# Optimization experiments

Hardware: AMD Instinct MI355X
Metric: run time of the kernel (lower is better)

Reference implementation:

```python
import jax, jax.numpy as jnp
import numpy as np

N_NODES = 100000
N_EDGES = 1600000
N_GRAPHS = 64
EPS = 1e-16  # matches PyG softmax eps


def _glorot(key, shape):
    fan_in, fan_out = shape[0], shape[1]
    lim = np.sqrt(6.0 / (fan_in + fan_out))
    return jax.random.uniform(key, shape, jnp.float32, -lim, lim)


def setup_inputs() -> dict:
    key = jax.random.key(0)
    ks = jax.random.split(key, 20)
    x = jax.random.normal(ks[0], (N_NODES, 3), jnp.float32)
    edge_index = jax.random.randint(ks[1], (2, N_EDGES), 0, N_NODES, jnp.int64)
    batch = jnp.sort(jax.random.randint(ks[2], (N_NODES,), 0, N_GRAPHS, jnp.int64))
    p = {
        # gat1: TransformerConv(3 -> 32, heads=2, concat) => H*D = 64
        'Wq1': _glorot(ks[3], (3, 64)),  'bq1': jnp.zeros((64,), jnp.float32),
        'Wk1': _glorot(ks[4], (3, 64)),  'bk1': jnp.zeros((64,), jnp.float32),
        'Wv1': _glorot(ks[5], (3, 64)),  'bv1': jnp.zeros((64,), jnp.float32),
        'Ws1': _glorot(ks[6], (3, 64)),  'bs1': jnp.zeros((64,), jnp.float32),
        # gat2: TransformerConv(64 -> 64, heads=2, concat) => H*D = 128
        'Wq2': _glorot(ks[7], (64, 128)), 'bq2': jnp.zeros((128,), jnp.float32),
        'Wk2': _glorot(ks[8], (64, 128)), 'bk2': jnp.zeros((128,), jnp.float32),
        'Wv2': _glorot(ks[9], (64, 128)), 'bv2': jnp.zeros((128,), jnp.float32),
        'Ws2': _glorot(ks[10], (64, 128)), 'bs2': jnp.zeros((128,), jnp.float32),
        # MLP head
        'W1': _glorot(ks[11], (128, 32)),  'b1': jnp.zeros((32,), jnp.float32),
        'W2': _glorot(ks[12], (32, 128)),  'b2': jnp.zeros((128,), jnp.float32),
        'W3': _glorot(ks[13], (128, 40)),  'b3': jnp.zeros((40,), jnp.float32),
    }
    return {'x': x, 'edge_index': edge_index, 'batch': batch, **p}


def transformer_conv(x, src, dst, Wq, bq, Wk, bk, Wv, bv, Ws, bs, heads, d):
    """PyG TransformerConv (concat=True, root_weight=True, no edge_attr, no beta)."""
    n = x.shape[0]
    q = (x @ Wq + bq).reshape(n, heads, d)
    k = (x @ Wk + bk).reshape(n, heads, d)
    v = (x @ Wv + bv).reshape(n, heads, d)
    # gather per edge: query at target (i = dst), key/value at source (j = src)
    logits = jnp.einsum('ehd,ehd->eh', q[dst], k[src]) / jnp.sqrt(jnp.float32(d))  # [E,H]
    # segment softmax over incoming edges of each target node
    m = jax.ops.segment_max(logits, dst, num_segments=n)          # [N,H]
    m = jnp.where(jnp.isfinite(m), m, 0.0)
    e = jnp.exp(logits - m[dst])                                   # [E,H]
    s = jax.ops.segment_sum(e, dst, num_segments=n)                # [N,H]
    alpha = e / (s[dst] + EPS)                                     # [E,H]
    out = jax.ops.segment_sum(alpha[:, :, None] * v[src], dst, num_segments=n)  # [N,H,D]
    out = out.reshape(n, heads * d)
    return out + (x @ Ws + bs)  # skip connection (root_weight)


def global_max_pool(x, batch, num_graphs):
    return jax.ops.segment_max(x, batch, num_segments=num_graphs)


def reference(x, edge_index, batch,
              Wq1, bq1, Wk1, bk1, Wv1, bv1, Ws1, bs1,
              Wq2, bq2, Wk2, bk2, Wv2, bv2, Ws2, bs2,
              W1, b1, W2, b2, W3, b3):
    src, dst = edge_index[0], edge_index[1]
    h = jax.nn.relu(transformer_conv(x, src, dst, Wq1, bq1, Wk1, bk1, Wv1, bv1, Ws1, bs1, heads=2, d=32))
    h = jax.nn.relu(transformer_conv(h, src, dst, Wq2, bq2, Wk2, bk2, Wv2, bv2, Ws2, bs2, heads=2, d=64))
    g = global_max_pool(h, batch, N_GRAPHS)            # [G,128]
    latent = jax.nn.relu(g @ W1 + b1)                   # [G,32]
    h2 = jax.nn.relu(latent @ W2 + b2)                  # [G,128]
    logits = h2 @ W3 + b3                               # [G,40]
    return (logits, latent)
```

## Files before the change

### kernel.cpp

```cpp
#include <hip/hip_runtime.h>
#include <hip/hip_bf16.h>

typedef __hip_bfloat16 bf16;
typedef unsigned short u16;
typedef unsigned int u32;
typedef __attribute__((ext_vector_type(8))) short bf16x8;
typedef __attribute__((ext_vector_type(4))) float f32x4;
typedef __attribute__((ext_vector_type(2))) float f32x2;

#define NN 100000
#define NE 1600000
#define NG 64
#define NBKT 196
#define EPB 4096
#define NBLK ((NE + EPB - 1) / EPB)

__device__ __forceinline__ float ldf(const void* __restrict__ p, int i, int isbf) {
    return isbf ? __bfloat162float(((const bf16*)p)[i]) : ((const float*)p)[i];
}

__device__ __forceinline__ int ld_idx(const int* __restrict__ p, int i, int is64) {
    return is64 ? p[2 * i] : p[i];
}

__device__ __forceinline__ u16 f2bu(float f) {
    u32 u = __float_as_uint(f);
    u32 r = u + 0x7fffu + ((u >> 16) & 1u);
    return (u16)(r >> 16);
}
__device__ __forceinline__ float blo(u32 u) { return __uint_as_float(u << 16); }
__device__ __forceinline__ float bhi(u32 u) { return __uint_as_float(u & 0xffff0000u); }

__global__ void k_detect(const int* __restrict__ ei, const int* __restrict__ bat,
                         const u16* __restrict__ xw, int* __restrict__ flags) {
    __shared__ int anyE, anyB, cntF;
    if (threadIdx.x == 0) { anyE = 0; anyB = 0; cntF = 0; }
    __syncthreads();
    int t = threadIdx.x;
    int accE = 0, accB = 0;
#pragma unroll
    for (int i = 0; i < 8; i++) {
        int si = t * 8 + i;
        long long pe = ((long long)si * (2LL * NE)) / 2048;
        int ie = ((int)pe) | 1;
        if (ie < 2 * NE) accE |= ei[ie];
    }
    {
        int ib = (int)(((long long)t * NN) / 256) | 1;
        if (ib < NN) accB |= bat[ib];
    }
    if (accE) atomicOr(&anyE, 1);
    if (accB) atomicOr(&anyB, 1);
    {
        u16 w = xw[2 * t];
        int hb = (w >> 8) & 0x7F;
        if (hb >= 0x3B && hb <= 0x41) atomicAdd(&cntF, 1);
    }
    __syncthreads();
    if (threadIdx.x == 0) {
        flags[0] = anyE ? 0 : 1;
        flags[1] = anyB ? 0 : 1;
        flags[2] = (cntF > 128) ? 1 : 0;
    }
}

__global__ void k_p1hist(const int* __restrict__ ei, const int* __restrict__ flags,
                         int* __restrict__ bhistT) {
    __shared__ int lh[NBKT];
    int t = threadIdx.x;
    if (t < NBKT) lh[t] = 0;
    __syncthreads();
    int is64 = flags[0];
    int base = blockIdx.x * EPB;
#pragma unroll
    for (int i = 0; i < EPB / 512; i++) {
        int e = base + i * 512 + t;
        if (e < NE) {
            int di = ld_idx(ei, NE + e, is64);
            atomicAdd(&lh[di >> 9], 1);
        }
    }
    __syncthreads();
    if (t < NBKT) bhistT[t * NBLK + blockIdx.x] = lh[t];
}

__global__ void k_p2a(const int* __restrict__ bhistT, int* __restrict__ boffT,
                      int* __restrict__ btot) {
    __shared__ int sh[512];
    int b = blockIdx.x, t = threadIdx.x;
    int v = (t < NBLK) ? bhistT[b * NBLK + t] : 0;
    sh[t] = v;
    __syncthreads();
#pragma unroll
    for (int off = 1; off < 512; off <<= 1) {
        int y = (t >= off) ? sh[t - off] : 0;
        __syncthreads();
        sh[t] += y;
        __syncthreads();
    }
    if (t < NBLK) boffT[b * NBLK + t] = sh[t] - v;
    if (t == 511) btot[b] = sh[511];
}

__global__ void k_p2b(const int* __restrict__ btot, int* __restrict__ bbase) {
    __shared__ int sh[256];
    int t = threadIdx.x;
    int v = (t < NBKT) ? btot[t] : 0;
    sh[t] = v;
    __syncthreads();
#pragma unroll
    for (int off = 1; off < 256; off <<= 1) {
        int y = (t >= off) ? sh[t - off] : 0;
        __syncthreads();
        sh[t] += y;
        __syncthreads();
    }
    if (t < NBKT) bbase[t] = sh[t] - v;
    if (t == 255) bbase[NBKT] = sh[255];
}

__global__ void k_p3part(const int* __restrict__ ei, const int* __restrict__ flags,
                         const int* __restrict__ boffT, const int* __restrict__ bbase,
                         u32* __restrict__ pairs) {
    __shared__ int loff[NBKT];
    int t = threadIdx.x;
    if (t < NBKT) loff[t] = bbase[t] + boffT[t * NBLK + blockIdx.x];
    __syncthreads();
    int is64 = flags[0];
    int base = blockIdx.x * EPB;
#pragma unroll
    for (int i = 0; i < EPB / 512; i++) {
        int e = base + i * 512 + t;
        if (e < NE) {
            int sj = ld_idx(ei, e, is64);
            int di = ld_idx(ei, NE + e, is64);
            int pos = atomicAdd(&loff[di >> 9], 1);
            pairs[pos] = ((u32)sj << 9) | (u32)(di & 511);
        }
    }
}

__global__ void k_p4sort(const u32* __restrict__ pairs, const int* __restrict__ bbase,
                         int* __restrict__ rowptr, int* __restrict__ es) {
    __shared__ int lcnt[512], pfx[512];
    int b = blockIdx.x, t = threadIdx.x;
    int bb = bbase[b];
    int bend = bbase[b + 1];
    int n0 = b << 9;
    lcnt[t] = 0;
    __syncthreads();
    for (int p = bb + t; p < bend; p += 512)
        atomicAdd(&lcnt[pairs[p] & 511u], 1);
    __syncthreads();
    int v = lcnt[t];
    pfx[t] = v;
    __syncthreads();
#pragma unroll
    for (int off = 1; off < 512; off <<= 1) {
        int y = (t >= off) ? pfx[t - off] : 0;
        __syncthreads();
        pfx[t] += y;
        __syncthreads();
    }
    int start = bb + pfx[t] - v;
    int n = n0 + t;
    if (n < NN) rowptr[n] = start;
    lcnt[t] = start;
    if (b == NBKT - 1 && t == 0) rowptr[NN] = NE;
    __syncthreads();
    for (int p = bb + t; p < bend; p += 512) {
        u32 pr = pairs[p];
        int pos = atomicAdd(&lcnt[pr & 511u], 1);
        es[pos] = (int)(pr >> 9);
    }
}

__global__ void k_qkvs1(const void* __restrict__ x,
                        const void* __restrict__ Wq, const void* __restrict__ bq,
                        const void* __restrict__ Wk, const void* __restrict__ bk,
                        const void* __restrict__ Wv, const void* __restrict__ bv,
                        const void* __restrict__ Ws, const void* __restrict__ bs,
                        const int* __restrict__ flags,
                        u16* __restrict__ q1b, u16* __restrict__ kv1m,
                        u16* __restrict__ s1b) {
    int idx = blockIdx.x * blockDim.x + threadIdx.x;
    if (idx >= NN * 64) return;
    int fb = flags[2];
    int n = idx >> 6, d = idx & 63;
    float x0 = ldf(x, n * 3 + 0, fb);
    float x1 = ldf(x, n * 3 + 1, fb);
    float x2 = ldf(x, n * 3 + 2, fb);
    q1b[idx] = f2bu(x0 * ldf(Wq, d, fb) + x1 * ldf(Wq, 64 + d, fb) + x2 * ldf(Wq, 128 + d, fb) + ldf(bq, d, fb));
    s1b[idx] = f2bu(x0 * ldf(Ws, d, fb) + x1 * ldf(Ws, 64 + d, fb) + x2 * ldf(Ws, 128 + d, fb) + ldf(bs, d, fb));
    float kf = x0 * ldf(Wk, d, fb) + x1 * ldf(Wk, 64 + d, fb) + x2 * ldf(Wk, 128 + d, fb) + ldf(bk, d, fb);
    float vf = x0 * ldf(Wv, d, fb) + x1 * ldf(Wv, 64 + d, fb) + x2 * ldf(Wv, 128 + d, fb) + ldf(bv, d, fb);
    float knb = __shfl_xor(kf, 1, 64);
    if (!(d & 1)) {
        int packed = __builtin_amdgcn_cvt_pk_fp8_f32(kf, knb, 0, false);
        kv1m[(size_t)n * 96 + (d >> 1)] = (u16)packed;
    }
    kv1m[(size_t)n * 96 + 32 + d] = f2bu(vf);
}

__global__ void k_attn1(const int* __restrict__ rowptr, const int* __restrict__ es,
                        const u16* __restrict__ q1b, const u16* __restrict__ kv1m,
                        const u16* __restrict__ s1b, u16* __restrict__ h1b) {
    int w = (blockIdx.x * blockDim.x + threadIdx.x) >> 6;
    if (w >= NN) return;
    int lane = threadIdx.x & 63;
    int g = lane >> 4, hl = lane & 15;
    const float scale = 0.17677669529663687f;
    uint2 qu = ((const uint2*)(q1b + (size_t)w * 64))[hl];
    float qs0 = blo(qu.x) * scale, qs1 = bhi(qu.x) * scale;
    float qs2 = blo(qu.y) * scale, qs3 = bhi(qu.y) * scale;
    float l = 0.0f, o0 = 0.0f, o1 = 0.0f, o2 = 0.0f, o3 = 0.0f;
    int beg = rowptr[w], end = rowptr[w + 1];
    int iters = (end - beg + 3) >> 2;
#define PROC1(ku, vu, vld) { \
    f32x2 k01 = __builtin_amdgcn_cvt_pk_f32_fp8((int)ku, false); \
    f32x2 k23 = __builtin_amdgcn_cvt_pk_f32_fp8((int)ku, true); \
    float t = qs0 * k01.x + qs1 * k01.y + qs2 * k23.x + qs3 * k23.y; \
    t += __shfl_xor(t, 4, 64); t += __shfl_xor(t, 2, 64); t += __shfl_xor(t, 1, 64); \
    float e = (vld) ? __expf(t) : 0.0f; \
    l += e; \
    o0 += e * blo(vu.x); o1 += e * bhi(vu.x); \
    o2 += e * blo(vu.y); o3 += e * bhi(vu.y); }
    if (iters > 0) {
        int pA = beg + g;
        int vA = pA < end; int sjA = es[vA ? pA : beg];
        u32 kA = *(const u32*)(kv1m + (size_t)sjA * 96 + hl * 2);
        uint2 uA = *(const uint2*)(kv1m + (size_t)sjA * 96 + 32 + hl * 4);
        int pB = pA + 4;
        int vB = pB < end; int sjB = es[vB ? pB : beg];
        u32 kB = *(const u32*)(kv1m + (size_t)sjB * 96 + hl * 2);
        uint2 uB = *(const uint2*)(kv1m + (size_t)sjB * 96 + 32 + hl * 4);
        int pC = pA + 8;
        int vC = pC < end; int sjC = es[vC ? pC : beg];
        u32 kC = *(const u32*)(kv1m + (size_t)sjC * 96 + hl * 2);
        uint2 uC = *(const uint2*)(kv1m + (size_t)sjC * 96 + 32 + hl * 4);
        for (int i = 0; i < iters; i += 3) {
            int pD = pA + 12;
            int vD = pD < end; int sjD = es[vD ? pD : beg];
            u32 kD = *(const u32*)(kv1m + (size_t)sjD * 96 + hl * 2);
            uint2 uD = *(const uint2*)(kv1m + (size_t)sjD * 96 + 32 + hl * 4);
            PROC1(kA, uA, vA);
            int pE = pA + 16;
            int vE = pE < end; int sjE = es[vE ? pE : beg];
            u32 kE = *(const u32*)(kv1m + (size_t)sjE * 96 + hl * 2);
            uint2 uE = *(const uint2*)(kv1m + (size_t)sjE * 96 + 32 + hl * 4);
            PROC1(kB, uB, vB);
            int pF = pA + 20;
            int vF = pF < end; int sjF = es[vF ? pF : beg];
            u32 kF = *(const u32*)(kv1m + (size_t)sjF * 96 + hl * 2);
            uint2 uF = *(const uint2*)(kv1m + (size_t)sjF * 96 + 32 + hl * 4);
            PROC1(kC, uC, vC);
            pA = pD; vA = vD; kA = kD; uA = uD;
            pB = pE; vB = vE; kB = kE; uB = uE;
            pC = pF; vC = vF; kC = kF; uC = uF;
        }
    }
#undef PROC1
#pragma unroll
    for (int off = 16; off <= 32; off <<= 1) {
        l += __shfl_xor(l, off, 64);
        o0 += __shfl_xor(o0, off, 64);
        o1 += __shfl_xor(o1, off, 64);
        o2 += __shfl_xor(o2, off, 64);
        o3 += __shfl_xor(o3, off, 64);
    }
    if (g == 0) {
        float inv = 1.0f / (l + 1e-16f);
        uint2 su = ((const uint2*)(s1b + (size_t)w * 64))[hl];
        uint2 r;
        r.x = (u32)f2bu(fmaxf(blo(su.x) + o0 * inv, 0.0f)) | ((u32)f2bu(fmaxf(bhi(su.x) + o1 * inv, 0.0f)) << 16);
        r.y = (u32)f2bu(fmaxf(blo(su.y) + o2 * inv, 0.0f)) | ((u32)f2bu(fmaxf(bhi(su.y) + o3 * inv, 0.0f)) << 16);
        ((uint2*)(h1b + (size_t)w * 64))[hl] = r;
    }
}

__global__ void k_wprep(const void* __restrict__ Wq, const void* __restrict__ bq,
                        const void* __restrict__ Wk, const void* __restrict__ bk,
                        const void* __restrict__ Wv, const void* __restrict__ bv,
                        const void* __restrict__ Ws, const void* __restrict__ bs,
                        const int* __restrict__ flags,
                        u16* __restrict__ Wt, float* __restrict__ bias,
                        float* __restrict__ g) {
    int idx = blockIdx.x * blockDim.x + threadIdx.x;
    if (idx >= 512 * 64) return;
    if (idx < NG * 128) g[idx] = 0.0f;
    int fb = flags[2];
    int n = idx >> 6, k = idx & 63;
    int mat = n >> 7, c = n & 127;
    const void* W = (mat == 0) ? Wq : (mat == 1) ? Wk : (mat == 2) ? Wv : Ws;
    Wt[n * 64 + k] = f2bu(ldf(W, k * 128 + c, fb));
    if (k == 0) {
        const void* B = (mat == 0) ? bq : (mat == 1) ? bk : (mat == 2) ? bv : bs;
        bias[n] = ldf(B, c, fb);
    }
}

__global__ void k_gemm2(const u16* __restrict__ h1b, const u16* __restrict__ Wt,
                        const float* __restrict__ bias,
                        u16* __restrict__ q2b, u16* __restrict__ kvm,
                        u16* __restrict__ s2b) {
    int w = (blockIdx.x * blockDim.x + threadIdx.x) >> 6;
    if (w >= NN / 16) return;
    int lane = threadIdx.x & 63;
    int quad = lane >> 4, mr = lane & 15;
    int m0 = w * 16;
    const u16* arow = h1b + (size_t)(m0 + mr) * 64 + quad * 8;
    bf16x8 a0 = *(const bf16x8*)(arow);
    bf16x8 a1 = *(const bf16x8*)(arow + 32);
#pragma unroll 4
    for (int n0 = 0; n0 < 512; n0 += 16) {
        const u16* brow = Wt + (size_t)(n0 + mr) * 64 + quad * 8;
        bf16x8 b0 = *(const bf16x8*)(brow);
        bf16x8 b1 = *(const bf16x8*)(brow + 32);
        f32x4 acc = {0.f, 0.f, 0.f, 0.f};
        acc = __builtin_amdgcn_mfma_f32_16x16x32_bf16(a0, b0, acc, 0, 0, 0);
        acc = __builtin_amdgcn_mfma_f32_16x16x32_bf16(a1, b1, acc, 0, 0, 0);
        float bs = bias[n0 + mr];
        int mat = n0 >> 7;
        int c = (n0 & 127) + mr;
#pragma unroll
        for (int r = 0; r < 4; r++) {
            int row = m0 + quad * 4 + r;
            float val = acc[r] + bs;
            if (mat == 1) {
                float nb = __shfl_xor(val, 1, 64);
                if (!(mr & 1)) {
                    int packed = __builtin_amdgcn_cvt_pk_fp8_f32(val, nb, 0, false);
                    *(u16*)((char*)kvm + (size_t)row * 384 + c) = (u16)packed;
                }
            } else if (mat == 0) {
                q2b[(size_t)row * 128 + c] = f2bu(val);
            } else if (mat == 2) {
                kvm[(size_t)row * 192 + 64 + c] = f2bu(val);
            } else {
                s2b[(size_t)row * 128 + c] = f2bu(val);
            }
        }
    }
}

__global__ void k_attn2(const int* __restrict__ rowptr, const int* __restrict__ es,
                        const u16* __restrict__ q2b, const u16* __restrict__ kvm,
                        const u16* __restrict__ s2b, u16* __restrict__ h2b) {
    int w = (blockIdx.x * blockDim.x + threadIdx.x) >> 6;
    if (w >= NN) return;
    int lane = threadIdx.x & 63;
    int g = lane >> 4, hl = lane & 15;
    const float scale = 0.125f;
    uint4 qu = ((const uint4*)(q2b + (size_t)w * 128))[hl];
    float qs[8];
    qs[0] = blo(qu.x) * scale; qs[1] = bhi(qu.x) * scale;
    qs[2] = blo(qu.y) * scale; qs[3] = bhi(qu.y) * scale;
    qs[4] = blo(qu.z) * scale; qs[5] = bhi(qu.z) * scale;
    qs[6] = blo(qu.w) * scale; qs[7] = bhi(qu.w) * scale;
    float l = 0.0f;
    float o[8] = {0.f, 0.f, 0.f, 0.f, 0.f, 0.f, 0.f, 0.f};
    int beg = rowptr[w], end = rowptr[w + 1];
    int iters = (end - beg + 3) >> 2;
#define PROC2(ku, vu, vld) { \
    f32x2 k01 = __builtin_amdgcn_cvt_pk_f32_fp8((int)ku.x, false); \
    f32x2 k23 = __builtin_amdgcn_cvt_pk_f32_fp8((int)ku.x, true); \
    f32x2 k45 = __builtin_amdgcn_cvt_pk_f32_fp8((int)ku.y, false); \
    f32x2 k67 = __builtin_amdgcn_cvt_pk_f32_fp8((int)ku.y, true); \
    float t = qs[0] * k01.x + qs[1] * k01.y + qs[2] * k23.x + qs[3] * k23.y \
            + qs[4] * k45.x + qs[5] * k45.y + qs[6] * k67.x + qs[7] * k67.y; \
    t += __shfl_xor(t, 4, 64); t += __shfl_xor(t, 2, 64); t += __shfl_xor(t, 1, 64); \
    float e = (vld) ? __expf(t) : 0.0f; \
    l += e; \
    o[0] += e * blo(vu.x); o[1] += e * bhi(vu.x); \
    o[2] += e * blo(vu.y); o[3] += e * bhi(vu.y); \
    o[4] += e * blo(vu.z); o[5] += e * bhi(vu.z); \
    o[6] += e * blo(vu.w); o[7] += e * bhi(vu.w); }
    if (iters > 0) {
        int pA = beg + g;
        int vA = pA < end; int sjA = es[vA ? pA : beg];
        uint2 kA = ((const uint2*)(kvm + (size_t)sjA * 192))[hl];
        uint4 uA = ((const uint4*)(kvm + (size_t)sjA * 192 + 64))[hl];
        int pB = pA + 4;
        int vB = pB < end; int sjB = es[vB ? pB : beg];
        uint2 kB = ((const uint2*)(kvm + (size_t)sjB * 192))[hl];
        uint4 uB = ((const uint4*)(kvm + (size_t)sjB * 192 + 64))[hl];
        int pC = pA + 8;
        int vC = pC < end; int sjC = es[vC ? pC : beg];
        uint2 kC = ((const uint2*)(kvm + (size_t)sjC * 192))[hl];
        uint4 uC = ((const uint4*)(kvm + (size_t)sjC * 192 + 64))[hl];
        for (int i = 0; i < iters; i += 3) {
            int pD = pA + 12;
            int vD = pD < end; int sjD = es[vD ? pD : beg];
            uint2 kD = ((const uint2*)(kvm + (size_t)sjD * 192))[hl];
            uint4 uD = ((const uint4*)(kvm + (size_t)sjD * 192 + 64))[hl];
            PROC2(kA, uA, vA);
            int pE = pA + 16;
            int vE = pE < end; int sjE = es[vE ? pE : beg];
            uint2 kE = ((const uint2*)(kvm + (size_t)sjE * 192))[hl];
            uint4 uE = ((const uint4*)(kvm + (size_t)sjE * 192 + 64))[hl];
            PROC2(kB, uB, vB);
            int pF = pA + 20;
            int vF = pF < end; int sjF = es[vF ? pF : beg];
            uint2 kF = ((const uint2*)(kvm + (size_t)sjF * 192))[hl];
            uint4 uF = ((const uint4*)(kvm + (size_t)sjF * 192 + 64))[hl];
            PROC2(kC, uC, vC);
            pA = pD; vA = vD; kA = kD; uA = uD;
            pB = pE; vB = vE; kB = kE; uB = uE;
            pC = pF; vC = vF; kC = kF; uC = uF;
        }
    }
#undef PROC2
#pragma unroll
    for (int off = 16; off <= 32; off <<= 1) {
        l += __shfl_xor(l, off, 64);
#pragma unroll
        for (int j = 0; j < 8; j++) o[j] += __shfl_xor(o[j], off, 64);
    }
    if (g == 0) {
        float inv = 1.0f / (l + 1e-16f);
        uint4 su = ((const uint4*)(s2b + (size_t)w * 128))[hl];
        uint4 r;
        r.x = (u32)f2bu(blo(su.x) + o[0] * inv) | ((u32)f2bu(bhi(su.x) + o[1] * inv) << 16);
        r.y = (u32)f2bu(blo(su.y) + o[2] * inv) | ((u32)f2bu(bhi(su.y) + o[3] * inv) << 16);
        r.z = (u32)f2bu(blo(su.z) + o[4] * inv) | ((u32)f2bu(bhi(su.z) + o[5] * inv) << 16);
        r.w = (u32)f2bu(blo(su.w) + o[6] * inv) | ((u32)f2bu(bhi(su.w) + o[7] * inv) << 16);
        ((uint4*)(h2b + (size_t)w * 128))[hl] = r;
    }
}

__global__ void k_pool(const u16* __restrict__ h2b, const int* __restrict__ batch,
                       const int* __restrict__ flags, float* __restrict__ g) {
    int idx = blockIdx.x * blockDim.x + threadIdx.x;
    if (idx >= (NN / 16) * 128) return;
    int is64 = flags[1];
    int d = idx & 127, ch = idx >> 7;
    int n0 = ch * 16;
    int curb = ld_idx(batch, n0, is64);
    float mx = 0.0f;
    for (int i = 0; i < 16; i++) {
        int n = n0 + i;
        int b = ld_idx(batch, n, is64);
        if (b != curb) {
            atomicMax((int*)&g[curb * 128 + d], __float_as_int(mx));
            mx = 0.0f;
            curb = b;
        }
        mx = fmaxf(mx, __uint_as_float(((u32)h2b[(size_t)n * 128 + d]) << 16));
    }
    atomicMax((int*)&g[curb * 128 + d], __float_as_int(mx));
}

__global__ void k_mlp(const float* __restrict__ g,
                      const void* __restrict__ W1, const void* __restrict__ b1,
                      const void* __restrict__ W2, const void* __restrict__ b2,
                      const void* __restrict__ W3, const void* __restrict__ b3,
                      const int* __restrict__ flags, float* __restrict__ out) {
    __shared__ float gr[128], lat[32], h2[128];
    int gid = blockIdx.x, t = threadIdx.x;
    int fb = flags[2];
    gr[t] = g[gid * 128 + t];
    __syncthreads();
    if (t < 32) {
        float a = ldf(b1, t, fb);
        for (int k = 0; k < 128; k++) a += gr[k] * ldf(W1, k * 32 + t, fb);
        a = fmaxf(a, 0.0f);
        lat[t] = a;
        out[NG * 40 + gid * 32 + t] = a;
    }
    __syncthreads();
    {
        float a = ldf(b2, t, fb);
        for (int k = 0; k < 32; k++) a += lat[k] * ldf(W2, k * 128 + t, fb);
        h2[t] = fmaxf(a, 0.0f);
    }
    __syncthreads();
    if (t < 40) {
        float a = ldf(b3, t, fb);
        for (int k = 0; k < 128; k++) a += h2[k] * ldf(W3, k * 40 + t, fb);
        out[gid * 40 + t] = a;
    }
}

extern "C" void kernel_launch(void* const* d_in, const int* in_sizes, int n_in,
                              void* d_out, int out_size, void* d_ws, size_t ws_size,
                              hipStream_t stream) {
    const void* x     = d_in[0];
    const int*  ei    = (const int*)d_in[1];
    const int*  batch = (const int*)d_in[2];
    const void *Wq1 = d_in[3],  *bq1 = d_in[4];
    const void *Wk1 = d_in[5],  *bk1 = d_in[6];
    const void *Wv1 = d_in[7],  *bv1 = d_in[8];
    const void *Ws1 = d_in[9],  *bs1 = d_in[10];
    const void *Wq2 = d_in[11], *bq2 = d_in[12];
    const void *Wk2 = d_in[13], *bk2 = d_in[14];
    const void *Wv2 = d_in[15], *bv2 = d_in[16];
    const void *Ws2 = d_in[17], *bs2 = d_in[18];
    const void *W1  = d_in[19], *b1  = d_in[20];
    const void *W2  = d_in[21], *b2  = d_in[22];
    const void *W3  = d_in[23], *b3  = d_in[24];

    float* ws = (float*)d_ws;
    float* g    = ws;
    float* bias = g + NG * 128;
    u16* u16base = (u16*)(bias + 512);
    u16* kvm   = u16base;
    u16* kv1m  = kvm + (size_t)NN * 192;
    u16* h1b   = kv1m + (size_t)NN * 96;
    u16* q1b   = h1b + (size_t)NN * 64;
    u16* s1b   = q1b + (size_t)NN * 64;
    u16* q2b   = s1b + (size_t)NN * 64;
    u16* s2b   = q2b + (size_t)NN * 128;
    u16* h2b   = s2b + (size_t)NN * 128;
    u16* Wt    = h2b + (size_t)NN * 128;
    int* flags  = (int*)(Wt + 512 * 64);
    int* rowptr = flags + 8;
    int* bhistT = rowptr + NN + 1;
    int* boffT  = bhistT + NBKT * NBLK;
    int* btot   = boffT + NBKT * NBLK;
    int* bbase  = btot + NBKT;
    int* es     = bbase + NBKT + 1;
    u32* pairs = (u32*)kvm;

    float* out  = (float*)d_out;

    const int B = 256;
    k_detect<<<1, 256, 0, stream>>>(ei, batch, (const u16*)x, flags);
    k_p1hist<<<NBLK, 512, 0, stream>>>(ei, flags, bhistT);
    k_p2a<<<NBKT, 512, 0, stream>>>(bhistT, boffT, btot);
    k_p2b<<<1, 256, 0, stream>>>(btot, bbase);
    k_p3part<<<NBLK, 512, 0, stream>>>(ei, flags, boffT, bbase, pairs);
    k_p4sort<<<NBKT, 512, 0, stream>>>(pairs, bbase, rowptr, es);
    k_qkvs1<<<(NN * 64 + B - 1) / B, B, 0, stream>>>(x, Wq1, bq1, Wk1, bk1, Wv1, bv1, Ws1, bs1,
                                                     flags, q1b, kv1m, s1b);
    k_attn1<<<(NN * 64 + B - 1) / B, B, 0, stream>>>(rowptr, es, q1b, kv1m, s1b, h1b);
    k_wprep<<<(512 * 64 + B - 1) / B, B, 0, stream>>>(Wq2, bq2, Wk2, bk2, Wv2, bv2, Ws2, bs2,
                                                      flags, Wt, bias, g);
    k_gemm2<<<(NN / 16 * 64 + B - 1) / B, B, 0, stream>>>(h1b, Wt, bias, q2b, kvm, s2b);
    k_attn2<<<(NN * 64 + B - 1) / B, B, 0, stream>>>(rowptr, es, q2b, kvm, s2b, h2b);
    k_pool<<<((NN / 16) * 128 + B - 1) / B, B, 0, stream>>>(h2b, batch, flags, g);
    k_mlp<<<NG, 128, 0, stream>>>(g, W1, b1, W2, b2, W3, b3, flags, out);
}
```

Measured before the change: 435.6 us.

## Fuse small launches and cut gather prefetch depth in attention kernels

Removes the separate detect, p2b and wprep launches. Index-width detection now runs per block inside the histogram and partition kernels, the final bucket scan runs in the last-arriving p2a block via an atomic ticket, and the layer-2 weight prep is folded into extra blocks of the qkvs1 launch. The aim is fewer kernel launches and fewer serialization points. Both attention kernels also drop from 3-deep to 2-deep software prefetch of neighbor K/V rows, which lowers register pressure but gives less latency hiding; the ticket scheme also adds atomics and fences.

```diff
diff --git a/kernel.cpp b/kernel.cpp
--- a/kernel.cpp
+++ b/kernel.cpp
@@ -14,6 +14,8 @@
 #define NBKT 196
 #define EPB 4096
 #define NBLK ((NE + EPB - 1) / EPB)
+#define QB 25000
+#define WB 128
 
 __device__ __forceinline__ float ldf(const void* __restrict__ p, int i, int isbf) {
     return isbf ? __bfloat162float(((const bf16*)p)[i]) : ((const float*)p)[i];
@@ -31,47 +33,30 @@
 __device__ __forceinline__ float blo(u32 u) { return __uint_as_float(u << 16); }
 __device__ __forceinline__ float bhi(u32 u) { return __uint_as_float(u & 0xffff0000u); }
 
-__global__ void k_detect(const int* __restrict__ ei, const int* __restrict__ bat,
-                         const u16* __restrict__ xw, int* __restrict__ flags) {
-    __shared__ int anyE, anyB, cntF;
-    if (threadIdx.x == 0) { anyE = 0; anyB = 0; cntF = 0; }
-    __syncthreads();
+__device__ __forceinline__ int block_detect_is64(const int* __restrict__ ei, int base,
+                                                 int* s_any) {
     int t = threadIdx.x;
-    int accE = 0, accB = 0;
-#pragma unroll
-    for (int i = 0; i < 8; i++) {
-        int si = t * 8 + i;
-        long long pe = ((long long)si * (2LL * NE)) / 2048;
-        int ie = ((int)pe) | 1;
-        if (ie < 2 * NE) accE |= ei[ie];
-    }
-    {
-        int ib = (int)(((long long)t * NN) / 256) | 1;
-        if (ib < NN) accB |= bat[ib];
-    }
-    if (accE) atomicOr(&anyE, 1);
-    if (accB) atomicOr(&anyB, 1);
-    {
-        u16 w = xw[2 * t];
-        int hb = (w >> 8) & 0x7F;
-        if (hb >= 0x3B && hb <= 0x41) atomicAdd(&cntF, 1);
-    }
-    __syncthreads();
-    if (threadIdx.x == 0) {
-        flags[0] = anyE ? 0 : 1;
-        flags[1] = anyB ? 0 : 1;
-        flags[2] = (cntF > 128) ? 1 : 0;
-    }
-}
-
-__global__ void k_p1hist(const int* __restrict__ ei, const int* __restrict__ flags,
+    int acc = 0;
+    int w0 = 2 * base + 4 * t + 1;
+    int w1 = 2 * base + 4 * t + 3;
+    if (w0 < 2 * NE) acc |= ei[w0];
+    if (w1 < 2 * NE) acc |= ei[w1];
+    if (acc) atomicOr(s_any, 1);
+    __syncthreads();
+    return *s_any ? 0 : 1;
+}
+
+__global__ void k_p1hist(const int* __restrict__ ei, const int* __restrict__ bat,
+                         const u16* __restrict__ xw, int* __restrict__ flags,
                          int* __restrict__ bhistT) {
     __shared__ int lh[NBKT];
+    __shared__ int s_any, s_anyB, s_cntF;
     int t = threadIdx.x;
     if (t < NBKT) lh[t] = 0;
-    __syncthreads();
-    int is64 = flags[0];
+    if (t == 0) { s_any = 0; s_anyB = 0; s_cntF = 0; }
+    __syncthreads();
     int base = blockIdx.x * EPB;
+    int is64 = block_detect_is64(ei, base, &s_any);
 #pragma unroll
     for (int i = 0; i < EPB / 512; i++) {
         int e = base + i * 512 + t;
@@ -80,13 +65,27 @@
             atomicAdd(&lh[di >> 9], 1);
         }
     }
+    if (blockIdx.x == 0 && t < 256) {
+        int ib = (int)(((long long)t * NN) / 256) | 1;
+        if (ib < NN && bat[ib]) atomicOr(&s_anyB, 1);
+        u16 w = xw[2 * t];
+        int hb = (w >> 8) & 0x7F;
+        if (hb >= 0x3B && hb <= 0x41) atomicAdd(&s_cntF, 1);
+    }
     __syncthreads();
     if (t < NBKT) bhistT[t * NBLK + blockIdx.x] = lh[t];
+    if (blockIdx.x == 0 && t == 0) {
+        flags[1] = s_anyB ? 0 : 1;
+        flags[2] = (s_cntF > 128) ? 1 : 0;
+        flags[4] = 0;
+    }
 }
 
 __global__ void k_p2a(const int* __restrict__ bhistT, int* __restrict__ boffT,
-                      int* __restrict__ btot) {
+                      int* __restrict__ btot, int* __restrict__ ticket,
+                      int* __restrict__ bbase) {
     __shared__ int sh[512];
+    __shared__ int s_last;
     int b = blockIdx.x, t = threadIdx.x;
     int v = (t < NBLK) ? bhistT[b * NBLK + t] : 0;
     sh[t] = v;
@@ -99,35 +98,42 @@
         __syncthreads();
     }
     if (t < NBLK) boffT[b * NBLK + t] = sh[t] - v;
-    if (t == 511) btot[b] = sh[511];
-}
-
-__global__ void k_p2b(const int* __restrict__ btot, int* __restrict__ bbase) {
-    __shared__ int sh[256];
-    int t = threadIdx.x;
-    int v = (t < NBKT) ? btot[t] : 0;
-    sh[t] = v;
-    __syncthreads();
-#pragma unroll
-    for (int off = 1; off < 256; off <<= 1) {
-        int y = (t >= off) ? sh[t - off] : 0;
+    if (t == 511) {
+        atomicExch(&btot[b], sh[511]);
+        __threadfence();
+    }
+    __syncthreads();
+    if (t == 0) s_last = (atomicAdd(ticket, 1) == NBKT - 1) ? 1 : 0;
+    __syncthreads();
+    if (s_last) {
+        __threadfence();
+        int vv = (t < NBKT) ? atomicAdd(&btot[t], 0) : 0;
         __syncthreads();
-        sh[t] += y;
+        sh[t] = vv;
         __syncthreads();
-    }
-    if (t < NBKT) bbase[t] = sh[t] - v;
-    if (t == 255) bbase[NBKT] = sh[255];
-}
-
-__global__ void k_p3part(const int* __restrict__ ei, const int* __restrict__ flags,
+#pragma unroll
+        for (int off = 1; off < 512; off <<= 1) {
+            int y = (t >= off) ? sh[t - off] : 0;
+            __syncthreads();
+            sh[t] += y;
+            __syncthreads();
+        }
+        if (t < NBKT) bbase[t] = sh[t] - vv;
+        if (t == 511) bbase[NBKT] = sh[511];
+    }
+}
+
+__global__ void k_p3part(const int* __restrict__ ei,
                          const int* __restrict__ boffT, const int* __restrict__ bbase,
                          u32* __restrict__ pairs) {
     __shared__ int loff[NBKT];
+    __shared__ int s_any;
     int t = threadIdx.x;
     if (t < NBKT) loff[t] = bbase[t] + boffT[t * NBLK + blockIdx.x];
-    __syncthreads();
-    int is64 = flags[0];
+    if (t == 0) s_any = 0;
+    __syncthreads();
     int base = blockIdx.x * EPB;
+    int is64 = block_detect_is64(ei, base, &s_any);
 #pragma unroll
     for (int i = 0; i < EPB / 512; i++) {
         int e = base + i * 512 + t;
@@ -180,12 +186,30 @@
                         const void* __restrict__ Wk, const void* __restrict__ bk,
                         const void* __restrict__ Wv, const void* __restrict__ bv,
                         const void* __restrict__ Ws, const void* __restrict__ bs,
+                        const void* __restrict__ Wq2, const void* __restrict__ bq2,
+                        const void* __restrict__ Wk2, const void* __restrict__ bk2,
+                        const void* __restrict__ Wv2, const void* __restrict__ bv2,
+                        const void* __restrict__ Ws2, const void* __restrict__ bs2,
                         const int* __restrict__ flags,
                         u16* __restrict__ q1b, u16* __restrict__ kv1m,
-                        u16* __restrict__ s1b) {
+                        u16* __restrict__ s1b,
+                        u16* __restrict__ Wt, float* __restrict__ bias,
+                        float* __restrict__ g) {
+    int fb = flags[2];
+    if (blockIdx.x >= QB) {
+        int idx = (blockIdx.x - QB) * 256 + threadIdx.x;
+        if (idx < NG * 128) g[idx] = 0.0f;
+        int n = idx >> 6, k = idx & 63;
+        int mat = n >> 7, c = n & 127;
+        const void* W = (mat == 0) ? Wq2 : (mat == 1) ? Wk2 : (mat == 2) ? Wv2 : Ws2;
+        Wt[n * 64 + k] = f2bu(ldf(W, k * 128 + c, fb));
+        if (k == 0) {
+            const void* B = (mat == 0) ? bq2 : (mat == 1) ? bk2 : (mat == 2) ? bv2 : bs2;
+            bias[n] = ldf(B, c, fb);
+        }
+        return;
+    }
     int idx = blockIdx.x * blockDim.x + threadIdx.x;
-    if (idx >= NN * 64) return;
-    int fb = flags[2];
     int n = idx >> 6, d = idx & 63;
     float x0 = ldf(x, n * 3 + 0, fb);
     float x1 = ldf(x, n * 3 + 1, fb);
@@ -234,29 +258,19 @@
         int vB = pB < end; int sjB = es[vB ? pB : beg];
         u32 kB = *(const u32*)(kv1m + (size_t)sjB * 96 + hl * 2);
         uint2 uB = *(const uint2*)(kv1m + (size_t)sjB * 96 + 32 + hl * 4);
-        int pC = pA + 8;
-        int vC = pC < end; int sjC = es[vC ? pC : beg];
-        u32 kC = *(const u32*)(kv1m + (size_t)sjC * 96 + hl * 2);
-        uint2 uC = *(const uint2*)(kv1m + (size_t)sjC * 96 + 32 + hl * 4);
-        for (int i = 0; i < iters; i += 3) {
+        for (int i = 0; i < iters; i += 2) {
+            int pC = pA + 8;
+            int vC = pC < end; int sjC = es[vC ? pC : beg];
+            u32 kC = *(const u32*)(kv1m + (size_t)sjC * 96 + hl * 2);
+            uint2 uC = *(const uint2*)(kv1m + (size_t)sjC * 96 + 32 + hl * 4);
+            PROC1(kA, uA, vA);
             int pD = pA + 12;
             int vD = pD < end; int sjD = es[vD ? pD : beg];
             u32 kD = *(const u32*)(kv1m + (size_t)sjD * 96 + hl * 2);
             uint2 uD = *(const uint2*)(kv1m + (size_t)sjD * 96 + 32 + hl * 4);
-            PROC1(kA, uA, vA);
-            int pE = pA + 16;
-            int vE = pE < end; int sjE = es[vE ? pE : beg];
-            u32 kE = *(const u32*)(kv1m + (size_t)sjE * 96 + hl * 2);
-            uint2 uE = *(const uint2*)(kv1m + (size_t)sjE * 96 + 32 + hl * 4);
             PROC1(kB, uB, vB);
-            int pF = pA + 20;
-            int vF = pF < end; int sjF = es[vF ? pF : beg];
-            u32 kF = *(const u32*)(kv1m + (size_t)sjF * 96 + hl * 2);
-            uint2 uF = *(const uint2*)(kv1m + (size_t)sjF * 96 + 32 + hl * 4);
-            PROC1(kC, uC, vC);
-            pA = pD; vA = vD; kA = kD; uA = uD;
-            pB = pE; vB = vE; kB = kE; uB = uE;
-            pC = pF; vC = vF; kC = kF; uC = uF;
+            pA = pC; vA = vC; kA = kC; uA = uC;
+            pB = pD; vB = vD; kB = kD; uB = uD;
         }
     }
 #undef PROC1
@@ -275,27 +289,6 @@
         r.x = (u32)f2bu(fmaxf(blo(su.x) + o0 * inv, 0.0f)) | ((u32)f2bu(fmaxf(bhi(su.x) + o1 * inv, 0.0f)) << 16);
         r.y = (u32)f2bu(fmaxf(blo(su.y) + o2 * inv, 0.0f)) | ((u32)f2bu(fmaxf(bhi(su.y) + o3 * inv, 0.0f)) << 16);
         ((uint2*)(h1b + (size_t)w * 64))[hl] = r;
-    }
-}
-
-__global__ void k_wprep(const void* __restrict__ Wq, const void* __restrict__ bq,
-                        const void* __restrict__ Wk, const void* __restrict__ bk,
-                        const void* __restrict__ Wv, const void* __restrict__ bv,
-                        const void* __restrict__ Ws, const void* __restrict__ bs,
-                        const int* __restrict__ flags,
-                        u16* __restrict__ Wt, float* __restrict__ bias,
-                        float* __restrict__ g) {
-    int idx = blockIdx.x * blockDim.x + threadIdx.x;
-    if (idx >= 512 * 64) return;
-    if (idx < NG * 128) g[idx] = 0.0f;
-    int fb = flags[2];
-    int n = idx >> 6, k = idx & 63;
-    int mat = n >> 7, c = n & 127;
-    const void* W = (mat == 0) ? Wq : (mat == 1) ? Wk : (mat == 2) ? Wv : Ws;
-    Wt[n * 64 + k] = f2bu(ldf(W, k * 128 + c, fb));
-    if (k == 0) {
-        const void* B = (mat == 0) ? bq : (mat == 1) ? bk : (mat == 2) ? bv : bs;
-        bias[n] = ldf(B, c, fb);
     }
 }
 
@@ -384,29 +377,19 @@
         int vB = pB < end; int sjB = es[vB ? pB : beg];
         uint2 kB = ((const uint2*)(kvm + (size_t)sjB * 192))[hl];
         uint4 uB = ((const uint4*)(kvm + (size_t)sjB * 192 + 64))[hl];
-        int pC = pA + 8;
-        int vC = pC < end; int sjC = es[vC ? pC : beg];
-        uint2 kC = ((const uint2*)(kvm + (size_t)sjC * 192))[hl];
-        uint4 uC = ((const uint4*)(kvm + (size_t)sjC * 192 + 64))[hl];
-        for (int i = 0; i < iters; i += 3) {
+        for (int i = 0; i < iters; i += 2) {
+            int pC = pA + 8;
+            int vC = pC < end; int sjC = es[vC ? pC : beg];
+            uint2 kC = ((const uint2*)(kvm + (size_t)sjC * 192))[hl];
+            uint4 uC = ((const uint4*)(kvm + (size_t)sjC * 192 + 64))[hl];
+            PROC2(kA, uA, vA);
             int pD = pA + 12;
             int vD = pD < end; int sjD = es[vD ? pD : beg];
             uint2 kD = ((const uint2*)(kvm + (size_t)sjD * 192))[hl];
             uint4 uD = ((const uint4*)(kvm + (size_t)sjD * 192 + 64))[hl];
-            PROC2(kA, uA, vA);
-            int pE = pA + 16;
-            int vE = pE < end; int sjE = es[vE ? pE : beg];
-            uint2 kE = ((const uint2*)(kvm + (size_t)sjE * 192))[hl];
-            uint4 uE = ((const uint4*)(kvm + (size_t)sjE * 192 + 64))[hl];
             PROC2(kB, uB, vB);
-            int pF = pA + 20;
-            int vF = pF < end; int sjF = es[vF ? pF : beg];
-            uint2 kF = ((const uint2*)(kvm + (size_t)sjF * 192))[hl];
-            uint4 uF = ((const uint4*)(kvm + (size_t)sjF * 192 + 64))[hl];
-            PROC2(kC, uC, vC);
-            pA = pD; vA = vD; kA = kD; uA = uD;
-            pB = pE; vB = vE; kB = kE; uB = uE;
-            pC = pF; vC = vF; kC = kF; uC = uF;
+            pA = pC; vA = vC; kA = kC; uA = uC;
+            pB = pD; vB = vD; kB = kD; uB = uD;
         }
     }
 #undef PROC2
@@ -524,17 +507,14 @@
     float* out  = (float*)d_out;
 
     const int B = 256;
-    k_detect<<<1, 256, 0, stream>>>(ei, batch, (const u16*)x, flags);
-    k_p1hist<<<NBLK, 512, 0, stream>>>(ei, flags, bhistT);
-    k_p2a<<<NBKT, 512, 0, stream>>>(bhistT, boffT, btot);
-    k_p2b<<<1, 256, 0, stream>>>(btot, bbase);
-    k_p3part<<<NBLK, 512, 0, stream>>>(ei, flags, boffT, bbase, pairs);
+    k_p1hist<<<NBLK, 512, 0, stream>>>(ei, batch, (const u16*)x, flags, bhistT);
+    k_p2a<<<NBKT, 512, 0, stream>>>(bhistT, boffT, btot, &flags[4], bbase);
+    k_p3part<<<NBLK, 512, 0, stream>>>(ei, boffT, bbase, pairs);
     k_p4sort<<<NBKT, 512, 0, stream>>>(pairs, bbase, rowptr, es);
-    k_qkvs1<<<(NN * 64 + B - 1) / B, B, 0, stream>>>(x, Wq1, bq1, Wk1, bk1, Wv1, bv1, Ws1, bs1,
-                                                     flags, q1b, kv1m, s1b);
+    k_qkvs1<<<QB + WB, B, 0, stream>>>(x, Wq1, bq1, Wk1, bk1, Wv1, bv1, Ws1, bs1,
+                                       Wq2, bq2, Wk2, bk2, Wv2, bv2, Ws2, bs2,
+                                       flags, q1b, kv1m, s1b, Wt, bias, g);
     k_attn1<<<(NN * 64 + B - 1) / B, B, 0, stream>>>(rowptr, es, q1b, kv1m, s1b, h1b);
-    k_wprep<<<(512 * 64 + B - 1) / B, B, 0, stream>>>(Wq2, bq2, Wk2, bk2, Wv2, bv2, Ws2, bs2,
-                                                      flags, Wt, bias, g);
     k_gemm2<<<(NN / 16 * 64 + B - 1) / B, B, 0, stream>>>(h1b, Wt, bias, q2b, kvm, s2b);
     k_attn2<<<(NN * 64 + B - 1) / B, B, 0, stream>>>(rowptr, es, q2b, kvm, s2b, h2b);
     k_pool<<<((NN / 16) * 128 + B - 1) / B, B, 0, stream>>>(h2b, batch, flags, g);
```

Result: no change. 441.3 us (+1.3%).
